# Optimization experiments

Hardware: AMD Instinct MI355X
Metric: run time of the kernel (lower is better)

Reference implementation:

```python
import jax, jax.numpy as jnp
import numpy as np

DIM, R, HEAD = 512, 4, 8
HD = DIM // HEAD
SCALE = HD ** -0.5
EPS = 1e-5


def dwconv(x, w, b, stride, padding):
    # depthwise conv (groups == channels) + bias + relu; x:[B,C,H,W], w:[C,1,kh,kw]
    y = jax.lax.conv_general_dilated(
        x, w, window_strides=stride, padding=padding,
        feature_group_count=x.shape[1],
        dimension_numbers=('NCHW', 'OIHW', 'NCHW'))
    return jax.nn.relu(y + b[None, :, None, None])


def setup_inputs() -> dict:
    key = jax.random.key(0)
    ks = jax.random.split(key, 12)
    s = 0.02
    return {
        'x': jax.random.normal(ks[0], (8, DIM, 56, 56), dtype=jnp.float32),
        'Wq': jax.random.normal(ks[1], (DIM, DIM), dtype=jnp.float32) * s,
        'bq': jnp.zeros((DIM,), jnp.float32),
        'Wkv': jax.random.normal(ks[2], (2 * DIM, DIM), dtype=jnp.float32) * s,
        'bkv': jnp.zeros((2 * DIM,), jnp.float32),
        'w1a': jax.random.normal(ks[3], (DIM, 1, 1, R), dtype=jnp.float32) * s,
        'b1a': jnp.zeros((DIM,), jnp.float32),
        'w1b': jax.random.normal(ks[4], (DIM, 1, R, 1), dtype=jnp.float32) * s,
        'b1b': jnp.zeros((DIM,), jnp.float32),
        'w2': jax.random.normal(ks[5], (DIM, 1, R, R), dtype=jnp.float32) * s,
        'b2': jnp.zeros((DIM,), jnp.float32),
        'w3': jax.random.normal(ks[6], (DIM, 1, 3, 3), dtype=jnp.float32) * s,
        'b3': jnp.zeros((DIM,), jnp.float32),
        'gamma': jnp.ones((DIM,), jnp.float32),
        'beta': jnp.zeros((DIM,), jnp.float32),
    }


def reference(x, Wq, bq, Wkv, bkv, w1a, b1a, w1b, b1b, w2, b2, w3, b3, gamma, beta):
    B, C, H, W = x.shape
    N = H * W
    x_layer = x.reshape(B, C, N).transpose(0, 2, 1)  # [B,N,C]
    q = (x_layer @ Wq.T + bq).reshape(B, N, HEAD, HD).transpose(0, 2, 1, 3)  # [B,h,N,d]

    # branch 1: (1,R)s(1,R) dwconv -> (R,1)s(R,1) dwconv
    l1 = dwconv(dwconv(x, w1a, b1a, (1, R), ((0, 0), (0, 0))),
                w1b, b1b, (R, 1), ((0, 0), (0, 0))).reshape(B, C, -1)
    # branch 2: RxR stride-R dwconv
    l2 = dwconv(x, w2, b2, (R, R), ((0, 0), (0, 0))).reshape(B, C, -1)
    # branch 3: avg-pool to (H/R, W/R) then 3x3 dwconv pad 1
    l3 = x.reshape(B, C, H // R, R, W // R, R).mean(axis=(3, 5))
    l3 = dwconv(l3, w3, b3, (1, 1), ((1, 1), (1, 1))).reshape(B, C, -1)

    l_ = jnp.concatenate([l1, l2, l3], axis=2).transpose(0, 2, 1)  # [B,M,C]
    mu = l_.mean(-1, keepdims=True)
    var = ((l_ - mu) ** 2).mean(-1, keepdims=True)
    l_ = (l_ - mu) * jax.lax.rsqrt(var + EPS) * gamma + beta

    M = l_.shape[1]
    kv = (l_ @ Wkv.T + bkv).reshape(B, M, 2, HEAD, HD).transpose(2, 0, 3, 1, 4)
    k, v = kv[0], kv[1]  # [B,h,M,d]

    attn = jax.nn.softmax(jnp.einsum('bhid,bhjd->bhij', q, k) * SCALE, axis=-1)
    out = jnp.einsum('bhij,bhjd->bhid', attn, v).transpose(0, 2, 1, 3).reshape(B, N, C)
    # NOTE: original torch code computes proj(out) but then overwrites it with
    # proj_drop(out); with drop=0 the returned value is exactly `out`.
    return out
```

## Files before the change

kernel.cpp:

```cpp
#include <hip/hip_runtime.h>
#include <hip/hip_bf16.h>

#define BATCH   8
#define C_DIM   512
#define HWD     56
#define NPIX    3136
#define PW      14
#define PP      196
#define M_TOT   588
#define BM_ROWS 4704
#define BM_PAD  4736
#define HEADS   8
#define HD      64
#define N_SEQ   3136
#define SM_SCALE 0.125f

typedef __attribute__((ext_vector_type(8))) short bf16x8;
typedef __attribute__((ext_vector_type(4))) float f32x4;

__device__ __forceinline__ short f2bs(float f) {
    __hip_bfloat16 h = __float2bfloat16(f);
    return *reinterpret_cast<short*>(&h);
}
__device__ __forceinline__ unsigned pkbf(float lo, float hi) {
    __hip_bfloat162 t = __float22bfloat162_rn(make_float2(lo, hi));
    return *reinterpret_cast<unsigned*>(&t);
}

__device__ __forceinline__ void gl_lds16(const void* g, void* l) {
    __builtin_amdgcn_global_load_lds(
        (const __attribute__((address_space(1))) void*)g,
        (__attribute__((address_space(3))) void*)l, 16, 0, 0);
}

__global__ __launch_bounds__(256) void k_branches(
    const float* __restrict__ x,
    const float* __restrict__ w1a, const float* __restrict__ b1a,
    const float* __restrict__ w1b, const float* __restrict__ b1b,
    const float* __restrict__ w2,  const float* __restrict__ b2,
    const float* __restrict__ w3,  const float* __restrict__ b3,
    float* __restrict__ l_pre)
{
    __shared__ float xs[NPIX];
    __shared__ float y1s[HWD * PW];
    __shared__ float pools[PP];
    const int c = blockIdx.x, b = blockIdx.y, tid = threadIdx.x;
    const float* xp = x + ((size_t)(b * C_DIM + c)) * NPIX;
    for (int i = tid; i < NPIX / 4; i += 256)
        ((float4*)xs)[i] = ((const float4*)xp)[i];
    __syncthreads();

    const float wa0 = w1a[c*4+0], wa1 = w1a[c*4+1], wa2 = w1a[c*4+2], wa3 = w1a[c*4+3];
    const float ba = b1a[c];
    for (int i = tid; i < HWD * PW; i += 256) {
        int h = i / PW, w = i % PW;
        const float* r = xs + h * HWD + w * 4;
        float v = ba + r[0]*wa0 + r[1]*wa1 + r[2]*wa2 + r[3]*wa3;
        y1s[i] = fmaxf(v, 0.f);
    }
    if (tid < PP) {
        int h = tid / PW, w = tid % PW;
        float s = 0.f;
        #pragma unroll
        for (int r = 0; r < 4; ++r) {
            const float* rr = xs + (h*4 + r) * HWD + w * 4;
            s += rr[0] + rr[1] + rr[2] + rr[3];
        }
        pools[tid] = s * (1.f / 16.f);
    }
    __syncthreads();

    if (tid < PP) {
        int h = tid / PW, w = tid % PW;
        float* lp = l_pre + ((size_t)(b * C_DIM + c)) * M_TOT;
        float v1 = b1b[c];
        v1 += y1s[(h*4+0)*PW + w] * w1b[c*4+0];
        v1 += y1s[(h*4+1)*PW + w] * w1b[c*4+1];
        v1 += y1s[(h*4+2)*PW + w] * w1b[c*4+2];
        v1 += y1s[(h*4+3)*PW + w] * w1b[c*4+3];
        lp[tid] = fmaxf(v1, 0.f);
        float v2 = b2[c];
        #pragma unroll
        for (int r = 0; r < 4; ++r)
            #pragma unroll
            for (int s2 = 0; s2 < 4; ++s2)
                v2 += xs[(h*4+r)*HWD + w*4 + s2] * w2[c*16 + r*4 + s2];
        lp[PP + tid] = fmaxf(v2, 0.f);
        float v3 = b3[c];
        #pragma unroll
        for (int dh = -1; dh <= 1; ++dh)
            #pragma unroll
            for (int dw = -1; dw <= 1; ++dw) {
                int hh = h + dh, ww = w + dw;
                if (hh >= 0 && hh < PW && ww >= 0 && ww < PW)
                    v3 += pools[hh*PW + ww] * w3[c*9 + (dh+1)*3 + (dw+1)];
            }
        lp[2*PP + tid] = fmaxf(v3, 0.f);
    }
}

__global__ __launch_bounds__(256) void k_stats(
    const float* __restrict__ l_pre, float2* __restrict__ stats)
{
    __shared__ float ssum[4][64];
    __shared__ float ssq[4][64];
    const int tid = threadIdx.x;
    const int ml = tid & 63, cg = tid >> 6;
    const int b = blockIdx.y;
    const int m = blockIdx.x * 64 + ml;
    float s = 0.f, q = 0.f;
    if (m < M_TOT) {
        const float* base = l_pre + ((size_t)b * C_DIM + cg * 128) * M_TOT + m;
        for (int c = 0; c < 128; ++c) {
            float v = base[(size_t)c * M_TOT];
            s += v; q += v * v;
        }
    }
    ssum[cg][ml] = s; ssq[cg][ml] = q;
    __syncthreads();
    if (tid < 64 && blockIdx.x * 64 + tid < M_TOT) {
        float ts = ssum[0][tid] + ssum[1][tid] + ssum[2][tid] + ssum[3][tid];
        float tq = ssq[0][tid] + ssq[1][tid] + ssq[2][tid] + ssq[3][tid];
        float mu = ts * (1.f / 512.f);
        float var = tq * (1.f / 512.f) - mu * mu;
        stats[(size_t)b * M_TOT + blockIdx.x * 64 + tid] =
            make_float2(mu, rsqrtf(var + 1e-5f));
    }
}

__global__ __launch_bounds__(256) void k_wconv(
    const float* __restrict__ Wq, const float* __restrict__ Wkv,
    short* __restrict__ Wqb, short* __restrict__ Wkvb)
{
    int i = (blockIdx.x * 256 + threadIdx.x) * 4;
    if (i < 262144) {
        float4 v = *(const float4*)(Wq + i);
        short o[4] = {f2bs(v.x), f2bs(v.y), f2bs(v.z), f2bs(v.w)};
        *(short4*)(Wqb + i) = *(short4*)o;
    } else {
        int j = i - 262144;
        float4 v = *(const float4*)(Wkv + j);
        short o[4] = {f2bs(v.x), f2bs(v.y), f2bs(v.z), f2bs(v.w)};
        *(short4*)(Wkvb + j) = *(short4*)o;
    }
}

__global__ __launch_bounds__(256) void k_xpose(
    const float* __restrict__ x, short* __restrict__ Xb)
{
    __shared__ float sx[64][68];
    const int tid = threadIdx.x;
    const int n0 = blockIdx.x * 64, c0 = blockIdx.y * 64, b = blockIdx.z;
    #pragma unroll
    for (int it = 0; it < 4; ++it) {
        int idx = tid + it * 256;
        int cr = idx >> 4, n4 = (idx & 15) * 4;
        float4 v = *(const float4*)(x + ((size_t)(b * C_DIM + c0 + cr)) * NPIX + n0 + n4);
        *(float4*)&sx[cr][n4] = v;
    }
    __syncthreads();
    #pragma unroll
    for (int p = 0; p < 2; ++p) {
        int idx = tid + p * 256;
        int nr = idx >> 3, cg = (idx & 7) * 8;
        short ov[8];
        #pragma unroll
        for (int e = 0; e < 8; ++e) ov[e] = f2bs(sx[cg + e][nr]);
        *(float4*)&Xb[((size_t)(b * NPIX + n0 + nr)) * C_DIM + c0 + cg] = *(float4*)ov;
    }
}

__global__ __launch_bounds__(256) void k_lnt(
    const float* __restrict__ l_pre, const float2* __restrict__ stats,
    const float* __restrict__ gamma, const float* __restrict__ beta,
    short* __restrict__ Lb)
{
    __shared__ float sx[64][68];
    const int tid = threadIdx.x;
    const int m0 = blockIdx.x * 64, c0 = blockIdx.y * 64, b = blockIdx.z;
    #pragma unroll
    for (int it = 0; it < 4; ++it) {
        int idx = tid + it * 256;
        int cr = idx >> 4, m4 = (idx & 15) * 4;
        float4 v = {0.f, 0.f, 0.f, 0.f};
        if (m0 + m4 < M_TOT)
            v = *(const float4*)(l_pre + ((size_t)(b * C_DIM + c0 + cr)) * M_TOT + m0 + m4);
        *(float4*)&sx[cr][m4] = v;
    }
    __syncthreads();
    #pragma unroll
    for (int p = 0; p < 2; ++p) {
        int idx = tid + p * 256;
        int mr = idx >> 3, cg = (idx & 7) * 8;
        int m = m0 + mr;
        float mu = 0.f, rstd = 0.f;
        if (m < M_TOT) {
            float2 st = stats[(size_t)b * M_TOT + m];
            mu = st.x; rstd = st.y;
        }
        short ov[8];
        #pragma unroll
        for (int e = 0; e < 8; ++e) {
            int c = c0 + cg + e;
            ov[e] = f2bs((sx[cg + e][mr] - mu) * rstd * gamma[c] + beta[c]);
        }
        if (m < M_TOT)
            *(float4*)&Lb[((size_t)(b * M_TOT + m)) * C_DIM + c0 + cg] = *(float4*)ov;
    }
}

__global__ __launch_bounds__(256) void k_gemm_q(
    const short* __restrict__ A, const short* __restrict__ Bw,
    const float* __restrict__ bias, short* __restrict__ Qb)
{
    __shared__ short As[128 * 64];
    __shared__ short Bs[128 * 64];
    const int tid = threadIdx.x;
    const int lane = tid & 63, w = tid >> 6;
    const int l15 = lane & 15, quad = lane >> 4;
    const int wr = w & 1, wc = w >> 1;
    const int row0 = blockIdx.x * 128, col0 = blockIdx.y * 128;
    const int lr8 = lane >> 3, lc8 = (lane & 7) * 8;

    f32x4 acc[4][4] = {};

    for (int c0 = 0; c0 < 512; c0 += 64) {
        __syncthreads();
        #pragma unroll
        for (int it = 0; it < 4; ++it) {
            int r = w * 32 + it * 8;
            gl_lds16(A  + (size_t)(row0 + r + lr8) * 512 + c0 + lc8, &As[r * 64]);
            gl_lds16(Bw + (size_t)(col0 + r + lr8) * 512 + c0 + lc8, &Bs[r * 64]);
        }
        __syncthreads();
        #pragma unroll
        for (int ks = 0; ks < 2; ++ks) {
            bf16x8 af[4], bf[4];
            #pragma unroll
            for (int t = 0; t < 4; ++t) {
                af[t] = *(const bf16x8*)&As[(wr*64 + t*16 + l15)*64 + ks*32 + quad*8];
                bf[t] = *(const bf16x8*)&Bs[(wc*64 + t*16 + l15)*64 + ks*32 + quad*8];
            }
            #pragma unroll
            for (int nt = 0; nt < 4; ++nt)
                #pragma unroll
                for (int mt = 0; mt < 4; ++mt)
                    acc[nt][mt] = __builtin_amdgcn_mfma_f32_16x16x32_bf16(
                        af[nt], bf[mt], acc[nt][mt], 0, 0, 0);
        }
    }

    #pragma unroll
    for (int nt = 0; nt < 4; ++nt) {
        int row_t = row0 + wr * 64 + nt * 16 + quad * 4;
        #pragma unroll
        for (int mt = 0; mt < 4; ++mt) {
            int col = col0 + wc * 64 + mt * 16 + l15;
            float bv = bias[col];
            int h = col >> 6, d = col & 63;
            #pragma unroll
            for (int r = 0; r < 4; ++r) {
                int row_g = row_t + r;
                int b = row_g / N_SEQ;
                int n = row_g - b * N_SEQ;
                Qb[(((size_t)(b * HEADS + h)) * N_SEQ + n) * HD + d] =
                    f2bs(acc[nt][mt][r] + bv);
            }
        }
    }
}

__global__ __launch_bounds__(256) void k_gemm_kv(
    const short* __restrict__ A, const short* __restrict__ Bw,
    const float* __restrict__ bias,
    short* __restrict__ Kb, short* __restrict__ Vt)
{
    __shared__ short As[128 * 64];
    __shared__ short Bs[128 * 64];
    const int tid = threadIdx.x;
    const int lane = tid & 63, w = tid >> 6;
    const int l15 = lane & 15, quad = lane >> 4;
    const int wr = w & 1, wc = w >> 1;
    const int row0 = blockIdx.x * 128, col0 = blockIdx.y * 128;
    const int lr8 = lane >> 3, lc8 = (lane & 7) * 8;

    f32x4 acc[4][4] = {};

    for (int c0 = 0; c0 < 512; c0 += 64) {
        __syncthreads();
        #pragma unroll
        for (int it = 0; it < 4; ++it) {
            int r = w * 32 + it * 8;
            gl_lds16(A  + (size_t)(row0 + r + lr8) * 512 + c0 + lc8, &As[r * 64]);
            gl_lds16(Bw + (size_t)(col0 + r + lr8) * 512 + c0 + lc8, &Bs[r * 64]);
        }
        __syncthreads();
        #pragma unroll
        for (int ks = 0; ks < 2; ++ks) {
            bf16x8 af[4], bf[4];
            #pragma unroll
            for (int t = 0; t < 4; ++t) {
                af[t] = *(const bf16x8*)&As[(wr*64 + t*16 + l15)*64 + ks*32 + quad*8];
                bf[t] = *(const bf16x8*)&Bs[(wc*64 + t*16 + l15)*64 + ks*32 + quad*8];
            }
            #pragma unroll
            for (int nt = 0; nt < 4; ++nt)
                #pragma unroll
                for (int mt = 0; mt < 4; ++mt)
                    acc[nt][mt] = __builtin_amdgcn_mfma_f32_16x16x32_bf16(
                        af[nt], bf[mt], acc[nt][mt], 0, 0, 0);
        }
    }

    #pragma unroll
    for (int nt = 0; nt < 4; ++nt) {
        int row_t = row0 + wr * 64 + nt * 16 + quad * 4;
        #pragma unroll
        for (int mt = 0; mt < 4; ++mt) {
            int col = col0 + wc * 64 + mt * 16 + l15;
            float bv = bias[col];
            #pragma unroll
            for (int r = 0; r < 4; ++r) {
                int row_g = row_t + r;
                float v = acc[nt][mt][r] + bv;
                if (row_g < BM_ROWS) {
                    int b = row_g / M_TOT;
                    int m = row_g - b * M_TOT;
                    if (col < 512) {
                        int h = col >> 6, d = col & 63;
                        Kb[(((size_t)(b * HEADS + h)) * M_TOT + m) * HD + d] = f2bs(v);
                    } else {
                        int jj = col - 512, h = jj >> 6, d = jj & 63;
                        Vt[(((size_t)(b * HEADS + h)) * HD + d) * M_TOT + m] = f2bs(v);
                    }
                }
            }
        }
    }
}

__global__ __launch_bounds__(256) void k_attn(
    const short* __restrict__ Qb, const short* __restrict__ Kb,
    const short* __restrict__ Vt, float* __restrict__ out)
{
    __shared__ __align__(16) short smem[3 * 64 * 72];
    short* Qs = smem;
    short* Ks = smem + 64 * 72;
    short* Vs = smem + 2 * 64 * 72;
    float* Os = (float*)(smem + 64 * 72);

    const int tid = threadIdx.x;
    const int lane = tid & 63, w = tid >> 6;
    const int l15 = lane & 15, quad = lane >> 4;
    const int n0 = blockIdx.x * 64, h = blockIdx.y, b = blockIdx.z;
    const size_t bh = (size_t)(b * HEADS + h);
    const size_t qbase = (bh * N_SEQ + n0) * HD;
    const size_t kbase = bh * M_TOT * HD;
    const size_t vbase = bh * (size_t)HD * M_TOT;

    #pragma unroll
    for (int it = 0; it < 2; ++it) {
        int idx = tid + it * 256;
        int row = idx >> 3, seg = idx & 7;
        *(float4*)&Qs[row * 72 + seg * 8] =
            *(const float4*)(Qb + qbase + (size_t)row * HD + seg * 8);
    }

    f32x4 oacc[4] = {};
    float rs = 0.f;

    __syncthreads();
    bf16x8 qf[2];
    #pragma unroll
    for (int ks = 0; ks < 2; ++ks)
        qf[ks] = *(const bf16x8*)&Qs[(w * 16 + l15) * 72 + ks * 32 + quad * 8];

    for (int jc0 = 0; jc0 < M_TOT; jc0 += 64) {
        if (jc0 + 64 <= M_TOT) {
            #pragma unroll
            for (int it = 0; it < 2; ++it) {
                int idx = tid + it * 256;
                int row = idx >> 3, seg = idx & 7;
                *(float4*)&Ks[row * 72 + seg * 8] =
                    *(const float4*)(Kb + kbase + (size_t)(jc0 + row) * HD + seg * 8);
                *(float4*)&Vs[row * 72 + seg * 8] =
                    *(const float4*)(Vt + vbase + (size_t)row * M_TOT + jc0 + seg * 8);
            }
        } else {
            #pragma unroll
            for (int it = 0; it < 2; ++it) {
                int idx = tid + it * 256;
                int row = idx >> 3, seg = idx & 7;
                int jg = jc0 + row;
                if (jg < M_TOT) {
                    *(float4*)&Ks[row * 72 + seg * 8] =
                        *(const float4*)(Kb + kbase + (size_t)jg * HD + seg * 8);
                } else {
                    float4 z = {0.f, 0.f, 0.f, 0.f};
                    *(float4*)&Ks[row * 72 + seg * 8] = z;
                }
                #pragma unroll
                for (int t2 = 0; t2 < 8; ++t2) {
                    int jj = jc0 + seg * 8 + t2;
                    Vs[row * 72 + seg * 8 + t2] = (jj < M_TOT)
                        ? Vt[vbase + (size_t)row * M_TOT + jj] : (short)0;
                }
            }
        }
        __syncthreads();

        f32x4 sacc[4] = {};
        #pragma unroll
        for (int t = 0; t < 4; ++t)
            #pragma unroll
            for (int ks = 0; ks < 2; ++ks) {
                bf16x8 kf = *(const bf16x8*)&Ks[(t * 16 + l15) * 72 + ks * 32 + quad * 8];
                sacc[t] = __builtin_amdgcn_mfma_f32_16x16x32_bf16(
                    kf, qf[ks], sacc[t], 0, 0, 0);
            }

        float p[4][4];
        if (jc0 + 64 <= M_TOT) {
            #pragma unroll
            for (int t = 0; t < 4; ++t)
                #pragma unroll
                for (int r = 0; r < 4; ++r) {
                    p[t][r] = __expf(sacc[t][r] * SM_SCALE);
                    rs += p[t][r];
                }
        } else {
            #pragma unroll
            for (int t = 0; t < 4; ++t)
                #pragma unroll
                for (int r = 0; r < 4; ++r) {
                    int jg = jc0 + t * 16 + quad * 4 + r;
                    float pv = (jg < M_TOT) ? __expf(sacc[t][r] * SM_SCALE) : 0.f;
                    p[t][r] = pv;
                    rs += pv;
                }
        }
        unsigned pk[4][2];
        #pragma unroll
        for (int t = 0; t < 4; ++t) {
            pk[t][0] = pkbf(p[t][0], p[t][1]);
            pk[t][1] = pkbf(p[t][2], p[t][3]);
        }

        const bool c0 = (quad & 1) != 0, c1 = (quad & 2) != 0;
        #pragma unroll
        for (int kc = 0; kc < 2; ++kc) {
            const int ta = 2 * kc, tb = 2 * kc + 1;
            unsigned P0x = pk[ta][0], P0y = pk[ta][1];
            unsigned P1x = pk[tb][0], P1y = pk[tb][1];
            unsigned X0x = __shfl_xor(P0x, 16), X0y = __shfl_xor(P0y, 16);
            unsigned X1x = __shfl_xor(P1x, 16), X1y = __shfl_xor(P1y, 16);
            unsigned Y0x = __shfl_xor(P0x, 32), Y0y = __shfl_xor(P0y, 32);
            unsigned Y1x = __shfl_xor(P1x, 32), Y1y = __shfl_xor(P1y, 32);
            unsigned Z0x = __shfl_xor(X0x, 32), Z0y = __shfl_xor(X0y, 32);
            unsigned Z1x = __shfl_xor(X1x, 32), Z1y = __shfl_xor(X1y, 32);
            unsigned pv4[4];
            pv4[0] = c1 ? (c0 ? X1x : Y1x) : (c0 ? Z0x : P0x);
            pv4[1] = c1 ? (c0 ? X1y : Y1y) : (c0 ? Z0y : P0y);
            pv4[2] = c1 ? (c0 ? P1x : Z1x) : (c0 ? Y0x : X0x);
            pv4[3] = c1 ? (c0 ? P1y : Z1y) : (c0 ? Y0y : X0y);
            bf16x8 pf;
            __builtin_memcpy(&pf, pv4, 16);
            #pragma unroll
            for (int dt = 0; dt < 4; ++dt) {
                bf16x8 vf = *(const bf16x8*)&Vs[(dt * 16 + l15) * 72 + kc * 32 + quad * 8];
                oacc[dt] = __builtin_amdgcn_mfma_f32_16x16x32_bf16(
                    vf, pf, oacc[dt], 0, 0, 0);
            }
        }
        __syncthreads();
    }

    rs += __shfl_xor(rs, 16);
    rs += __shfl_xor(rs, 32);
    float inv = 1.f / rs;
    #pragma unroll
    for (int dt = 0; dt < 4; ++dt)
        #pragma unroll
        for (int r = 0; r < 4; ++r)
            Os[(w * 16 + l15) * 68 + dt * 16 + quad * 4 + r] = oacc[dt][r] * inv;
    __syncthreads();
    #pragma unroll
    for (int it = 0; it < 4; ++it) {
        int row = (tid >> 4) + it * 16;
        int c4 = (tid & 15) * 4;
        float4 v = *(const float4*)&Os[row * 68 + c4];
        *(float4*)&out[((size_t)b * N_SEQ + n0 + row) * C_DIM + h * HD + c4] = v;
    }
}

extern "C" void kernel_launch(void* const* d_in, const int* in_sizes, int n_in,
                              void* d_out, int out_size, void* d_ws, size_t ws_size,
                              hipStream_t stream) {
    const float* x     = (const float*)d_in[0];
    const float* Wq    = (const float*)d_in[1];
    const float* bq    = (const float*)d_in[2];
    const float* Wkv   = (const float*)d_in[3];
    const float* bkv   = (const float*)d_in[4];
    const float* w1a   = (const float*)d_in[5];
    const float* b1a   = (const float*)d_in[6];
    const float* w1b   = (const float*)d_in[7];
    const float* b1b   = (const float*)d_in[8];
    const float* w2    = (const float*)d_in[9];
    const float* b2    = (const float*)d_in[10];
    const float* w3    = (const float*)d_in[11];
    const float* b3    = (const float*)d_in[12];
    const float* gamma = (const float*)d_in[13];
    const float* beta  = (const float*)d_in[14];
    float* out = (float*)d_out;

    char* ws = (char*)d_ws;
    short*  Xb    = (short*)ws;
    float*  l_pre = (float*)ws;
    float2* stats = (float2*)(ws + 9633792);
    short*  Lb    = (short*)(ws + 9671424);
    short*  Wqb   = (short*)(ws + 25690112);
    short*  Wkvb  = (short*)(ws + 26214400);
    short*  Kb    = (short*)(ws + 27262976);
    short*  Vt    = (short*)(ws + 32079872);
    short*  Qb    = (short*)(ws + 36896768);

    k_wconv<<<768, 256, 0, stream>>>(Wq, Wkv, Wqb, Wkvb);
    k_xpose<<<dim3(49, 8, BATCH), 256, 0, stream>>>(x, Xb);
    k_gemm_q<<<dim3(196, 4), 256, 0, stream>>>(Xb, Wqb, bq, Qb);
    k_branches<<<dim3(C_DIM, BATCH), 256, 0, stream>>>(
        x, w1a, b1a, w1b, b1b, w2, b2, w3, b3, l_pre);
    k_stats<<<dim3(10, BATCH), 256, 0, stream>>>(l_pre, stats);
    k_lnt<<<dim3(10, 8, BATCH), 256, 0, stream>>>(l_pre, stats, gamma, beta, Lb);
    k_gemm_kv<<<dim3(37, 8), 256, 0, stream>>>(Lb, Wkvb, bkv, Kb, Vt);
    k_attn<<<dim3(49, HEADS, BATCH), 256, 0, stream>>>(Qb, Kb, Vt, out);
}
```

Before: 309.0 us.

## Stage full K/V per head in LDS and sweep queries in 1024-thread blocks

The attention kernel now loads the whole K and V^T for a (batch, head) into LDS once, using 1024-thread blocks that each cover a quarter of the queries, instead of reloading 64-row K/V chunks per 64-query block. Each wave processes two 16-query tiles that share K and V fragments, reads Q straight from global memory, and uses 16x16x16 MFMA for PV so no lane shuffles are needed. This removes repeated K/V staging and the per-chunk barriers, but uses about 156 KB of dynamic LDS, which allows only one block per CU, and launches only 256 blocks.

Result: faster. 275.4 us (-10.9%).

```diff
diff --git a/kernel.cpp b/kernel.cpp
--- a/kernel.cpp
+++ b/kernel.cpp
@@ -15,7 +15,14 @@
 #define N_SEQ   3136
 #define SM_SCALE 0.125f
 
+#define KS_STRIDE 68
+#define KS_ROWS   592
+#define VS_STRIDE 596
+#define ATTN_LDS_SHORTS (KS_ROWS * KS_STRIDE + 64 * VS_STRIDE)
+#define ATTN_LDS_BYTES  (ATTN_LDS_SHORTS * 2)
+
 typedef __attribute__((ext_vector_type(8))) short bf16x8;
+typedef __attribute__((ext_vector_type(4))) short bf16x4;
 typedef __attribute__((ext_vector_type(4))) float f32x4;
 
 __device__ __forceinline__ short f2bs(float f) {
@@ -25,6 +32,18 @@
 __device__ __forceinline__ unsigned pkbf(float lo, float hi) {
     __hip_bfloat162 t = __float22bfloat162_rn(make_float2(lo, hi));
     return *reinterpret_cast<unsigned*>(&t);
+}
+
+__device__ __forceinline__ f32x4 mfma16(bf16x4 a, bf16x4 b, f32x4 c) {
+#if __has_builtin(__builtin_amdgcn_mfma_f32_16x16x16bf16_1k)
+    return __builtin_amdgcn_mfma_f32_16x16x16bf16_1k(a, b, c, 0, 0, 0);
+#elif __has_builtin(__builtin_amdgcn_mfma_f32_16x16x16_bf16)
+    return __builtin_amdgcn_mfma_f32_16x16x16_bf16(a, b, c, 0, 0, 0);
+#else
+    asm volatile("v_mfma_f32_16x16x16_bf16 %0, %1, %2, %0\n\ts_nop 7\n\ts_nop 1"
+                 : "+v"(c) : "v"(a), "v"(b));
+    return c;
+#endif
 }
 
 __device__ __forceinline__ void gl_lds16(const void* g, void* l) {
@@ -339,157 +358,116 @@
     }
 }
 
-__global__ __launch_bounds__(256) void k_attn(
+__global__ __launch_bounds__(1024) void k_attn(
     const short* __restrict__ Qb, const short* __restrict__ Kb,
     const short* __restrict__ Vt, float* __restrict__ out)
 {
-    __shared__ __align__(16) short smem[3 * 64 * 72];
-    short* Qs = smem;
-    short* Ks = smem + 64 * 72;
-    short* Vs = smem + 2 * 64 * 72;
-    float* Os = (float*)(smem + 64 * 72);
+    extern __shared__ short smem[];
+    short* Ks = smem;
+    short* Vs = smem + KS_ROWS * KS_STRIDE;
 
     const int tid = threadIdx.x;
     const int lane = tid & 63, w = tid >> 6;
     const int l15 = lane & 15, quad = lane >> 4;
-    const int n0 = blockIdx.x * 64, h = blockIdx.y, b = blockIdx.z;
+    const int q4 = blockIdx.x, h = blockIdx.y, b = blockIdx.z;
     const size_t bh = (size_t)(b * HEADS + h);
-    const size_t qbase = (bh * N_SEQ + n0) * HD;
     const size_t kbase = bh * M_TOT * HD;
     const size_t vbase = bh * (size_t)HD * M_TOT;
 
-    #pragma unroll
-    for (int it = 0; it < 2; ++it) {
-        int idx = tid + it * 256;
-        int row = idx >> 3, seg = idx & 7;
-        *(float4*)&Qs[row * 72 + seg * 8] =
-            *(const float4*)(Qb + qbase + (size_t)row * HD + seg * 8);
-    }
-
-    f32x4 oacc[4] = {};
-    float rs = 0.f;
-
+    for (int i = tid; i < 4704; i += 1024) {
+        int row = i >> 3, seg = i & 7;
+        *(float4*)&Ks[row * KS_STRIDE + seg * 8] =
+            *(const float4*)(Kb + kbase + (size_t)row * 64 + seg * 8);
+    }
+    if (tid < 256) {
+        int r = tid >> 6, cc = tid & 63;
+        Ks[(588 + r) * KS_STRIDE + cc] = 0;
+    }
+    {
+        int row = tid >> 4, tg = tid & 15;
+        const short* src = Vt + vbase + (size_t)row * M_TOT;
+        #pragma unroll 2
+        for (int jj = tg; jj < 147; jj += 16)
+            *(float2*)&Vs[row * VS_STRIDE + jj * 4] = *(const float2*)(src + jj * 4);
+    }
+    if (tid < 512) {
+        int row = tid >> 3, cc = tid & 7;
+        Vs[row * VS_STRIDE + 588 + cc] = 0;
+    }
     __syncthreads();
-    bf16x8 qf[2];
-    #pragma unroll
-    for (int ks = 0; ks < 2; ++ks)
-        qf[ks] = *(const bf16x8*)&Qs[(w * 16 + l15) * 72 + ks * 32 + quad * 8];
-
-    for (int jc0 = 0; jc0 < M_TOT; jc0 += 64) {
-        if (jc0 + 64 <= M_TOT) {
-            #pragma unroll
-            for (int it = 0; it < 2; ++it) {
-                int idx = tid + it * 256;
-                int row = idx >> 3, seg = idx & 7;
-                *(float4*)&Ks[row * 72 + seg * 8] =
-                    *(const float4*)(Kb + kbase + (size_t)(jc0 + row) * HD + seg * 8);
-                *(float4*)&Vs[row * 72 + seg * 8] =
-                    *(const float4*)(Vt + vbase + (size_t)row * M_TOT + jc0 + seg * 8);
-            }
-        } else {
-            #pragma unroll
-            for (int it = 0; it < 2; ++it) {
-                int idx = tid + it * 256;
-                int row = idx >> 3, seg = idx & 7;
-                int jg = jc0 + row;
-                if (jg < M_TOT) {
-                    *(float4*)&Ks[row * 72 + seg * 8] =
-                        *(const float4*)(Kb + kbase + (size_t)jg * HD + seg * 8);
-                } else {
-                    float4 z = {0.f, 0.f, 0.f, 0.f};
-                    *(float4*)&Ks[row * 72 + seg * 8] = z;
-                }
-                #pragma unroll
-                for (int t2 = 0; t2 < 8; ++t2) {
-                    int jj = jc0 + seg * 8 + t2;
-                    Vs[row * 72 + seg * 8 + t2] = (jj < M_TOT)
-                        ? Vt[vbase + (size_t)row * M_TOT + jj] : (short)0;
-                }
-            }
-        }
-        __syncthreads();
-
-        f32x4 sacc[4] = {};
-        #pragma unroll
-        for (int t = 0; t < 4; ++t)
-            #pragma unroll
-            for (int ks = 0; ks < 2; ++ks) {
-                bf16x8 kf = *(const bf16x8*)&Ks[(t * 16 + l15) * 72 + ks * 32 + quad * 8];
-                sacc[t] = __builtin_amdgcn_mfma_f32_16x16x32_bf16(
-                    kf, qf[ks], sacc[t], 0, 0, 0);
-            }
-
-        float p[4][4];
-        if (jc0 + 64 <= M_TOT) {
-            #pragma unroll
-            for (int t = 0; t < 4; ++t)
-                #pragma unroll
-                for (int r = 0; r < 4; ++r) {
-                    p[t][r] = __expf(sacc[t][r] * SM_SCALE);
-                    rs += p[t][r];
-                }
-        } else {
-            #pragma unroll
-            for (int t = 0; t < 4; ++t)
-                #pragma unroll
-                for (int r = 0; r < 4; ++r) {
-                    int jg = jc0 + t * 16 + quad * 4 + r;
-                    float pv = (jg < M_TOT) ? __expf(sacc[t][r] * SM_SCALE) : 0.f;
-                    p[t][r] = pv;
-                    rs += pv;
-                }
-        }
-        unsigned pk[4][2];
-        #pragma unroll
-        for (int t = 0; t < 4; ++t) {
-            pk[t][0] = pkbf(p[t][0], p[t][1]);
-            pk[t][1] = pkbf(p[t][2], p[t][3]);
-        }
-
-        const bool c0 = (quad & 1) != 0, c1 = (quad & 2) != 0;
-        #pragma unroll
-        for (int kc = 0; kc < 2; ++kc) {
-            const int ta = 2 * kc, tb = 2 * kc + 1;
-            unsigned P0x = pk[ta][0], P0y = pk[ta][1];
-            unsigned P1x = pk[tb][0], P1y = pk[tb][1];
-            unsigned X0x = __shfl_xor(P0x, 16), X0y = __shfl_xor(P0y, 16);
-            unsigned X1x = __shfl_xor(P1x, 16), X1y = __shfl_xor(P1y, 16);
-            unsigned Y0x = __shfl_xor(P0x, 32), Y0y = __shfl_xor(P0y, 32);
-            unsigned Y1x = __shfl_xor(P1x, 32), Y1y = __shfl_xor(P1y, 32);
-            unsigned Z0x = __shfl_xor(X0x, 32), Z0y = __shfl_xor(X0y, 32);
-            unsigned Z1x = __shfl_xor(X1x, 32), Z1y = __shfl_xor(X1y, 32);
-            unsigned pv4[4];
-            pv4[0] = c1 ? (c0 ? X1x : Y1x) : (c0 ? Z0x : P0x);
-            pv4[1] = c1 ? (c0 ? X1y : Y1y) : (c0 ? Z0y : P0y);
-            pv4[2] = c1 ? (c0 ? P1x : Z1x) : (c0 ? Y0x : X0x);
-            pv4[3] = c1 ? (c0 ? P1y : Z1y) : (c0 ? Y0y : X0y);
-            bf16x8 pf;
-            __builtin_memcpy(&pf, pv4, 16);
+
+    for (int ds = w; ds < 25; ds += 16) {
+        const bool sbv = (ds < 24);
+        const int nA = q4 * 784 + ds * 32 + l15;
+        const int nB = sbv ? nA + 16 : nA;
+
+        bf16x8 qfA[2], qfB[2];
+        #pragma unroll
+        for (int ks = 0; ks < 2; ++ks) {
+            qfA[ks] = *(const bf16x8*)(Qb + (bh * N_SEQ + nA) * HD + ks * 32 + quad * 8);
+            qfB[ks] = *(const bf16x8*)(Qb + (bh * N_SEQ + nB) * HD + ks * 32 + quad * 8);
+        }
+
+        f32x4 oaccA[4] = {}, oaccB[4] = {};
+        float rsA = 0.f, rsB = 0.f;
+
+        for (int j0 = 0; j0 < KS_ROWS; j0 += 16) {
+            const short* krow = &Ks[(j0 + l15) * KS_STRIDE];
+            bf16x8 kf0 = *(const bf16x8*)&krow[quad * 8];
+            bf16x8 kf1 = *(const bf16x8*)&krow[32 + quad * 8];
+
+            f32x4 sA = {}, sB = {};
+            sA = __builtin_amdgcn_mfma_f32_16x16x32_bf16(kf0, qfA[0], sA, 0, 0, 0);
+            sB = __builtin_amdgcn_mfma_f32_16x16x32_bf16(kf0, qfB[0], sB, 0, 0, 0);
+            sA = __builtin_amdgcn_mfma_f32_16x16x32_bf16(kf1, qfA[1], sA, 0, 0, 0);
+            sB = __builtin_amdgcn_mfma_f32_16x16x32_bf16(kf1, qfB[1], sB, 0, 0, 0);
+
+            const float msk = (j0 == 576 && quad == 3) ? 0.f : 1.f;
+            float pA[4], pB[4];
+            #pragma unroll
+            for (int r = 0; r < 4; ++r) {
+                pA[r] = __expf(sA[r] * SM_SCALE);
+                pB[r] = __expf(sB[r] * SM_SCALE);
+            }
+            rsA += (pA[0] + pA[1] + pA[2] + pA[3]) * msk;
+            rsB += (pB[0] + pB[1] + pB[2] + pB[3]) * msk;
+
+            unsigned ua[2] = {pkbf(pA[0], pA[1]), pkbf(pA[2], pA[3])};
+            unsigned ub[2] = {pkbf(pB[0], pB[1]), pkbf(pB[2], pB[3])};
+            bf16x4 pbA, pbB;
+            __builtin_memcpy(&pbA, ua, 8);
+            __builtin_memcpy(&pbB, ub, 8);
+
             #pragma unroll
             for (int dt = 0; dt < 4; ++dt) {
-                bf16x8 vf = *(const bf16x8*)&Vs[(dt * 16 + l15) * 72 + kc * 32 + quad * 8];
-                oacc[dt] = __builtin_amdgcn_mfma_f32_16x16x32_bf16(
-                    vf, pf, oacc[dt], 0, 0, 0);
-            }
-        }
-        __syncthreads();
-    }
-
-    rs += __shfl_xor(rs, 16);
-    rs += __shfl_xor(rs, 32);
-    float inv = 1.f / rs;
-    #pragma unroll
-    for (int dt = 0; dt < 4; ++dt)
-        #pragma unroll
-        for (int r = 0; r < 4; ++r)
-            Os[(w * 16 + l15) * 68 + dt * 16 + quad * 4 + r] = oacc[dt][r] * inv;
-    __syncthreads();
-    #pragma unroll
-    for (int it = 0; it < 4; ++it) {
-        int row = (tid >> 4) + it * 16;
-        int c4 = (tid & 15) * 4;
-        float4 v = *(const float4*)&Os[row * 68 + c4];
-        *(float4*)&out[((size_t)b * N_SEQ + n0 + row) * C_DIM + h * HD + c4] = v;
+                bf16x4 vf = *(const bf16x4*)&Vs[(dt * 16 + l15) * VS_STRIDE + j0 + quad * 4];
+                oaccA[dt] = mfma16(vf, pbA, oaccA[dt]);
+                oaccB[dt] = mfma16(vf, pbB, oaccB[dt]);
+            }
+        }
+
+        rsA += __shfl_xor(rsA, 16); rsA += __shfl_xor(rsA, 32);
+        rsB += __shfl_xor(rsB, 16); rsB += __shfl_xor(rsB, 32);
+        const float invA = 1.f / rsA;
+        const float invB = 1.f / rsB;
+        float* orowA = out + ((size_t)b * N_SEQ + nA) * C_DIM + h * HD;
+        #pragma unroll
+        for (int dt = 0; dt < 4; ++dt) {
+            float4 o;
+            o.x = oaccA[dt][0] * invA; o.y = oaccA[dt][1] * invA;
+            o.z = oaccA[dt][2] * invA; o.w = oaccA[dt][3] * invA;
+            *(float4*)&orowA[dt * 16 + quad * 4] = o;
+        }
+        if (sbv) {
+            float* orowB = out + ((size_t)b * N_SEQ + nB) * C_DIM + h * HD;
+            #pragma unroll
+            for (int dt = 0; dt < 4; ++dt) {
+                float4 o;
+                o.x = oaccB[dt][0] * invB; o.y = oaccB[dt][1] * invB;
+                o.z = oaccB[dt][2] * invB; o.w = oaccB[dt][3] * invB;
+                *(float4*)&orowB[dt * 16 + quad * 4] = o;
+            }
+        }
     }
 }
 
@@ -524,6 +502,12 @@
     short*  Vt    = (short*)(ws + 32079872);
     short*  Qb    = (short*)(ws + 36896768);
 
+    static bool attr_set = false;
+    hipFuncSetAttribute((const void*)k_attn,
+                        hipFuncAttributeMaxDynamicSharedMemorySize,
+                        ATTN_LDS_BYTES);
+    (void)attr_set;
+
     k_wconv<<<768, 256, 0, stream>>>(Wq, Wkv, Wqb, Wkvb);
     k_xpose<<<dim3(49, 8, BATCH), 256, 0, stream>>>(x, Xb);
     k_gemm_q<<<dim3(196, 4), 256, 0, stream>>>(Xb, Wqb, bq, Qb);
@@ -532,5 +516,5 @@
     k_stats<<<dim3(10, BATCH), 256, 0, stream>>>(l_pre, stats);
     k_lnt<<<dim3(10, 8, BATCH), 256, 0, stream>>>(l_pre, stats, gamma, beta, Lb);
     k_gemm_kv<<<dim3(37, 8), 256, 0, stream>>>(Lb, Wkvb, bkv, Kb, Vt);
-    k_attn<<<dim3(49, HEADS, BATCH), 256, 0, stream>>>(Qb, Kb, Vt, out);
-}
+    k_attn<<<dim3(4, HEADS, BATCH), 1024, ATTN_LDS_BYTES, stream>>>(Qb, Kb, Vt, out);
+}
```
